# Performance work log

Measured on AMD Instinct MI355X. Metric: run time of the kernel, lower is better.

The kernel has to match this reference:

```python
import jax, jax.numpy as jnp
import numpy as np

T, B, I, H, L = 512, 64, 1024, 1024, 2


def setup_inputs() -> dict:
    key = jax.random.key(0)
    ks = jax.random.split(key, 3)
    stdv = 1.0 / np.sqrt(H)
    x = jax.random.normal(ks[0], (T, B, I), dtype=jnp.float32)
    w_ih = jax.random.uniform(ks[1], (L, 4 * H, I), dtype=jnp.float32, minval=-stdv, maxval=stdv)
    w_hh = jax.random.uniform(ks[2], (L, 4 * H, H), dtype=jnp.float32, minval=-stdv, maxval=stdv)
    b_ih = jnp.zeros((L, 4 * H), dtype=jnp.float32)
    b_hh = jnp.zeros((L, 4 * H), dtype=jnp.float32)
    h0 = jnp.zeros((L, B, H), dtype=jnp.float32)
    c0 = jnp.zeros((L, B, H), dtype=jnp.float32)
    return {"x": x, "h0": h0, "c0": c0, "w_ih": w_ih, "w_hh": w_hh, "b_ih": b_ih, "b_hh": b_hh}


def _lstm_layer(seq, h, c, w_ih_l, w_hh_l, b_ih_l, b_hh_l):
    # in2hidden: one big GEMM over all timesteps, as in the torch code
    igates = jnp.einsum('tbi,gi->tbg', seq, w_ih_l) + b_ih_l  # (T, B, 4H)

    def step(carry, ig):
        h, c = carry
        gates = ig + h @ w_hh_l.T + b_hh_l          # (B, 4H)
        i_g, f_g, g_g, o_g = jnp.split(gates, 4, axis=-1)
        c = jax.nn.sigmoid(f_g) * c + jax.nn.sigmoid(i_g) * jnp.tanh(g_g)
        h = jax.nn.sigmoid(o_g) * jnp.tanh(c)
        return (h, c), h

    (hT, cT), out = jax.lax.scan(step, (h, c), igates)
    return out, hT, cT


def reference(x, h0, c0, w_ih, w_hh, b_ih, b_hh):
    out = x
    h_fin, c_fin = [], []
    for l in range(L):  # small fixed number of structurally distinct layers
        out, hT, cT = _lstm_layer(out, h0[l], c0[l], w_ih[l], w_hh[l], b_ih[l], b_hh[l])
        h_fin.append(hT)
        c_fin.append(cT)
    return out, jnp.stack(h_fin), jnp.stack(c_fin)
```

## Files before the change

kernel.cpp:

```cpp
#include <hip/hip_runtime.h>
#include <hip/hip_bf16.h>
#include <stdint.h>

#define T_STEPS 512
#define NBATCH 64
#define HID 1024
#define NGATE 4096
#define NLAYERS 2
#define BH (NBATCH * HID)
#define TBH (T_STEPS * NBATCH * HID)
#define WEL ((size_t)NLAYERS * NGATE * HID)
#define NBLK 256

typedef __attribute__((ext_vector_type(8))) short short8;
typedef __attribute__((ext_vector_type(4))) float f32x4;

__device__ __forceinline__ ushort f2bf(float f) {
  union { float f; uint32_t i; } u; u.f = f;
  return (ushort)((u.i + 0x7fffu + ((u.i >> 16) & 1u)) >> 16);
}
__device__ __forceinline__ float bf2f(ushort b) {
  union { uint32_t i; float f; } u; u.i = ((uint32_t)b) << 16;
  return u.f;
}
__device__ __forceinline__ void gll16(const void* g, void* l) {
  __builtin_amdgcn_global_load_lds(
      (const __attribute__((address_space(1))) unsigned int*)g,
      (__attribute__((address_space(3))) unsigned int*)l, 16, 0, 0);
}

#define ISSC(SLOT, PTR, OFF) \
  asm volatile("global_load_dwordx4 %0, %1, off offset:" #OFF \
               : "=v"(fr[SLOT]) : "v"(PTR));
#define ISSU(SLOT, PTR, OFF) \
  asm volatile("global_load_dwordx4 %0, %1, off offset:" #OFF " sc0 sc1" \
               : "=v"(fr[SLOT]) : "v"(PTR));
#define VMW(N, SLOT) \
  asm volatile("s_waitcnt vmcnt(" #N ")" : "+v"(fr[SLOT]));
#define CON(SLOT, KC) { \
    const short8 b0v = *(const short8*)(bb0 + ((((KC) * 64) + kb) ^ bsw)); \
    const short8 b1v = *(const short8*)(bb1 + ((((KC) * 64) + kb) ^ bsw)); \
    accA = __builtin_amdgcn_mfma_f32_16x16x32_bf16(fr[SLOT], b0v, accA, 0, 0, 0); \
    accB = __builtin_amdgcn_mfma_f32_16x16x32_bf16(fr[SLOT], b1v, accB, 0, 0, 0); }

#define PIPE64(M0, M1) \
  M0(0,A0p,0)    M0(1,A0p,64)   M0(2,A0p,128)  M0(3,A0p,192)  \
  M0(4,A0p,256)  M0(5,A0p,320)  M0(6,A0p,384)  M0(7,A0p,448)  \
  M0(8,A0p,512)  M0(9,A0p,576)  M0(10,A0p,640) M0(11,A0p,704) \
  M0(12,A0p,768) M0(13,A0p,832) M0(14,A0p,896) M0(15,A0p,960) \
  VMW(15,0)  CON(0,0)   M0(0,A0p,1024)  \
  VMW(15,1)  CON(1,1)   M0(1,A0p,1088)  \
  VMW(15,2)  CON(2,2)   M0(2,A0p,1152)  \
  VMW(15,3)  CON(3,3)   M0(3,A0p,1216)  \
  VMW(15,4)  CON(4,4)   M0(4,A0p,1280)  \
  VMW(15,5)  CON(5,5)   M0(5,A0p,1344)  \
  VMW(15,6)  CON(6,6)   M0(6,A0p,1408)  \
  VMW(15,7)  CON(7,7)   M0(7,A0p,1472)  \
  VMW(15,8)  CON(8,8)   M0(8,A0p,1536)  \
  VMW(15,9)  CON(9,9)   M0(9,A0p,1600)  \
  VMW(15,10) CON(10,10) M0(10,A0p,1664) \
  VMW(15,11) CON(11,11) M0(11,A0p,1728) \
  VMW(15,12) CON(12,12) M0(12,A0p,1792) \
  VMW(15,13) CON(13,13) M0(13,A0p,1856) \
  VMW(15,14) CON(14,14) M0(14,A0p,1920) \
  VMW(15,15) CON(15,15) M0(15,A0p,1984) \
  VMW(15,0)  CON(0,16)  M1(0,A1p,0)     \
  VMW(15,1)  CON(1,17)  M1(1,A1p,64)    \
  VMW(15,2)  CON(2,18)  M1(2,A1p,128)   \
  VMW(15,3)  CON(3,19)  M1(3,A1p,192)   \
  VMW(15,4)  CON(4,20)  M1(4,A1p,256)   \
  VMW(15,5)  CON(5,21)  M1(5,A1p,320)   \
  VMW(15,6)  CON(6,22)  M1(6,A1p,384)   \
  VMW(15,7)  CON(7,23)  M1(7,A1p,448)   \
  VMW(15,8)  CON(8,24)  M1(8,A1p,512)   \
  VMW(15,9)  CON(9,25)  M1(9,A1p,576)   \
  VMW(15,10) CON(10,26) M1(10,A1p,640)  \
  VMW(15,11) CON(11,27) M1(11,A1p,704)  \
  VMW(15,12) CON(12,28) M1(12,A1p,768)  \
  VMW(15,13) CON(13,29) M1(13,A1p,832)  \
  VMW(15,14) CON(14,30) M1(14,A1p,896)  \
  VMW(15,15) CON(15,31) M1(15,A1p,960)  \
  VMW(15,0)  CON(0,32)  M1(0,A1p,1024)  \
  VMW(15,1)  CON(1,33)  M1(1,A1p,1088)  \
  VMW(15,2)  CON(2,34)  M1(2,A1p,1152)  \
  VMW(15,3)  CON(3,35)  M1(3,A1p,1216)  \
  VMW(15,4)  CON(4,36)  M1(4,A1p,1280)  \
  VMW(15,5)  CON(5,37)  M1(5,A1p,1344)  \
  VMW(15,6)  CON(6,38)  M1(6,A1p,1408)  \
  VMW(15,7)  CON(7,39)  M1(7,A1p,1472)  \
  VMW(15,8)  CON(8,40)  M1(8,A1p,1536)  \
  VMW(15,9)  CON(9,41)  M1(9,A1p,1600)  \
  VMW(15,10) CON(10,42) M1(10,A1p,1664) \
  VMW(15,11) CON(11,43) M1(11,A1p,1728) \
  VMW(15,12) CON(12,44) M1(12,A1p,1792) \
  VMW(15,13) CON(13,45) M1(13,A1p,1856) \
  VMW(15,14) CON(14,46) M1(14,A1p,1920) \
  VMW(15,15) CON(15,47) M1(15,A1p,1984) \
  VMW(15,0)  CON(0,48)  \
  VMW(14,1)  CON(1,49)  \
  VMW(13,2)  CON(2,50)  \
  VMW(12,3)  CON(3,51)  \
  VMW(11,4)  CON(4,52)  \
  VMW(10,5)  CON(5,53)  \
  VMW(9,6)   CON(6,54)  \
  VMW(8,7)   CON(7,55)  \
  VMW(7,8)   CON(8,56)  \
  VMW(6,9)   CON(9,57)  \
  VMW(5,10)  CON(10,58) \
  VMW(4,11)  CON(11,59) \
  VMW(3,12)  CON(12,60) \
  VMW(2,13)  CON(13,61) \
  VMW(1,14)  CON(14,62) \
  VMW(0,15)  CON(15,63)

__global__ void k_f32_to_bf16(const float* __restrict__ in, ushort* __restrict__ out, int n) {
  int i = (blockIdx.x * blockDim.x + threadIdx.x) * 4;
  if (i >= n) return;
  const float4 v = *reinterpret_cast<const float4*>(in + i);
  ushort4 o; o.x = f2bf(v.x); o.y = f2bf(v.y); o.z = f2bf(v.z); o.w = f2bf(v.w);
  *reinterpret_cast<ushort4*>(out + i) = o;
}
__global__ void k_zero(int* p, int n) {
  int i = blockIdx.x * blockDim.x + threadIdx.x;
  if (i < n) p[i] = 0;
}

struct ScanP {
  const ushort* wih; const ushort* whh;
  const ushort* xb;  const ushort* hinit;
  ushort* h0r;
  ushort* h1d;
  const float* c0; const float* bi; const float* bh;
  float* out; int* bar;
};

__device__ __forceinline__ void gbar(int* bar, int phase, int stripe, bool isRoot) {
  __syncthreads();
  if (threadIdx.x == 0) {
    __hip_atomic_fetch_add(bar + stripe * 16, 1, __ATOMIC_RELAXED, __HIP_MEMORY_SCOPE_AGENT);
    if (isRoot) {
      const int target = (phase + 1) * NBLK;
      for (;;) {
        int sum = 0;
#pragma unroll
        for (int i = 0; i < 16; ++i)
          sum += __hip_atomic_load(bar + i * 16, __ATOMIC_RELAXED, __HIP_MEMORY_SCOPE_AGENT);
        if (sum >= target) break;
        __builtin_amdgcn_s_sleep(1);
      }
      __hip_atomic_store(bar + 256, phase + 1, __ATOMIC_RELAXED, __HIP_MEMORY_SCOPE_AGENT);
    } else {
      while (__hip_atomic_load(bar + 256, __ATOMIC_RELAXED, __HIP_MEMORY_SCOPE_AGENT) < phase + 1)
        __builtin_amdgcn_s_sleep(4);
    }
  }
  __syncthreads();
  __builtin_amdgcn_sched_barrier(0);
}

__global__ __launch_bounds__(256, 1) void k_scan(ScanP p) {
  __shared__ __align__(16) ushort Wl[32 * 2048];
  __shared__ float glds[64 * 33];
  const int tid = threadIdx.x, wave = tid >> 6, lane = tid & 63;
  const bool isL1 = blockIdx.x >= 128;
  const int cb = isL1 ? (int)blockIdx.x - 128 : (int)blockIdx.x;
  const int j0 = cb * 8;
  const int stripe = blockIdx.x & 15;
  const bool isRoot = (blockIdx.x == 0);

  const ushort* wihL = p.wih + (isL1 ? (size_t)NGATE * HID : 0);
  const ushort* whhL = p.whh + (isL1 ? (size_t)NGATE * HID : 0);
  for (int q = wave; q < 128; q += 4) {
    const int i = q >> 2, ch = q & 3;
    const ushort* base = (ch < 2) ? wihL : whhL;
    const int g = (i >> 3) * 1024 + j0 + (i & 7);
    gll16(base + (size_t)g * 1024 + (ch & 1) * 512 + (((lane * 16) ^ ((i & 7) << 4)) >> 1),
          (char*)Wl + i * 4096 + ch * 1024);
  }

  const int eb  = tid >> 2;
  const int jl0 = (tid & 3) * 2;
  const int jj  = j0 + jl0;
  const int lofs = isL1 ? NGATE : 0;
  float creg[2], bias[4][2];
#pragma unroll
  for (int i = 0; i < 2; ++i) creg[i] = p.c0[(isL1 ? BH : 0) + eb * 1024 + jj + i];
#pragma unroll
  for (int g = 0; g < 4; ++g)
#pragma unroll
    for (int i = 0; i < 2; ++i)
      bias[g][i] = p.bi[lofs + g * 1024 + jj + i] + p.bh[lofs + g * 1024 + jj + i];

  const size_t aoff = (size_t)(wave * 16 + (lane & 15)) * 1024 + (size_t)((lane >> 4) * 8);
  const int r0 = lane & 15;
  const char* bb0 = (const char*)Wl + r0 * 4096;
  const char* bb1 = (const char*)Wl + (r0 + 16) * 4096;
  const int bsw = (r0 & 7) << 4;
  const int kb = (lane >> 4) * 16;

  __syncthreads();

  for (int s = 0; s < T_STEPS + 1; ++s) {
    const bool act = isL1 ? (s >= 1) : (s < T_STEPS);
    if (act) {
      f32x4 accA = {0.f, 0.f, 0.f, 0.f}, accB = {0.f, 0.f, 0.f, 0.f};
      short8 fr[16];
      if (!isL1) {
        const ushort* A0p = p.xb + (size_t)s * BH + aoff;
        const ushort* A1p = ((s == 0) ? p.hinit : p.h0r + (size_t)(s - 1) * BH) + aoff;
        PIPE64(ISSC, ISSC)
      } else {
        const ushort* A0p = p.h0r + (size_t)(s - 1) * BH + aoff;
        const ushort* A1p = ((s == 1) ? p.hinit + BH : p.h1d + (size_t)(s & 1) * BH) + aoff;
        PIPE64(ISSC, ISSU)
      }
#pragma unroll
      for (int r = 0; r < 4; ++r) {
        const int row = wave * 16 + (lane >> 4) * 4 + r;
        glds[row * 33 + r0]      = accA[r];
        glds[row * 33 + 16 + r0] = accB[r];
      }
      __syncthreads();

      float hres[2];
#pragma unroll
      for (int i = 0; i < 2; ++i) {
        const int jl = jl0 + i;
        const float gi = glds[eb * 33 + jl]      + bias[0][i];
        const float gf = glds[eb * 33 + 8 + jl]  + bias[1][i];
        const float gg = glds[eb * 33 + 16 + jl] + bias[2][i];
        const float go = glds[eb * 33 + 24 + jl] + bias[3][i];
        float c = creg[i];
        const float si = 1.f / (1.f + __expf(-gi));
        const float sf = 1.f / (1.f + __expf(-gf));
        const float so = 1.f / (1.f + __expf(-go));
        const float tg = tanhf(gg);
        c = sf * c + si * tg;
        hres[i] = so * tanhf(c);
        creg[i] = c;
      }

      const uint32_t packed = (uint32_t)f2bf(hres[0]) | ((uint32_t)f2bf(hres[1]) << 16);
      ushort* hdst = (!isL1) ? (p.h0r + (size_t)s * BH)
                             : (p.h1d + (size_t)((s - 1) & 1) * BH);
      uint32_t* hw = (uint32_t*)(hdst + eb * 1024 + jj);
      __hip_atomic_store(hw, packed, __ATOMIC_RELAXED, __HIP_MEMORY_SCOPE_AGENT);
      uint32_t chk = __hip_atomic_load(hw, __ATOMIC_RELAXED, __HIP_MEMORY_SCOPE_AGENT);
      asm volatile("" :: "v"(chk));

      if (isL1) {
#pragma unroll
        for (int i = 0; i < 2; ++i)
          p.out[(size_t)(s - 1) * BH + eb * 1024 + jj + i] = hres[i];
        if (s - 1 == T_STEPS - 1) {
#pragma unroll
          for (int i = 0; i < 2; ++i) {
            p.out[(size_t)TBH + BH + eb * 1024 + jj + i] = hres[i];
            p.out[(size_t)TBH + 3 * BH + eb * 1024 + jj + i] = creg[i];
          }
        }
      } else if (s == T_STEPS - 1) {
#pragma unroll
        for (int i = 0; i < 2; ++i) {
          p.out[(size_t)TBH + eb * 1024 + jj + i] = hres[i];
          p.out[(size_t)TBH + 2 * BH + eb * 1024 + jj + i] = creg[i];
        }
      }
    }
    gbar(p.bar, s, stripe, isRoot);
  }
}

extern "C" void kernel_launch(void* const* d_in, const int* in_sizes, int n_in,
                              void* d_out, int out_size, void* d_ws, size_t ws_size,
                              hipStream_t stream) {
  const float* x    = (const float*)d_in[0];
  const float* h0   = (const float*)d_in[1];
  const float* c0   = (const float*)d_in[2];
  const float* w_ih = (const float*)d_in[3];
  const float* w_hh = (const float*)d_in[4];
  const float* b_ih = (const float*)d_in[5];
  const float* b_hh = (const float*)d_in[6];
  float* out = (float*)d_out;

  ushort* xb    = (ushort*)d_ws;
  ushort* wihb  = xb + (size_t)TBH;
  ushort* whhb  = wihb + WEL;
  ushort* hinit = whhb + WEL;
  ushort* h0r   = hinit + 2 * (size_t)BH;
  ushort* h1d   = h0r + (size_t)TBH;
  int*    bar   = (int*)(h1d + 2 * (size_t)BH);

  const size_t need = ((size_t)2 * TBH + 2 * WEL + 4 * (size_t)BH) * 2 + 4096;
  if (ws_size < need) return;

  { int n = TBH;        k_f32_to_bf16<<<(n / 4 + 255) / 256, 256, 0, stream>>>(x, xb, n); }
  { int n = (int)WEL;   k_f32_to_bf16<<<(n / 4 + 255) / 256, 256, 0, stream>>>(w_ih, wihb, n); }
  { int n = (int)WEL;   k_f32_to_bf16<<<(n / 4 + 255) / 256, 256, 0, stream>>>(w_hh, whhb, n); }
  { int n = 2 * BH;     k_f32_to_bf16<<<(n / 4 + 255) / 256, 256, 0, stream>>>(h0, hinit, n); }
  k_zero<<<2, 256, 0, stream>>>(bar, 512);

  ScanP sp;
  sp.wih = wihb; sp.whh = whhb;
  sp.xb = xb; sp.hinit = hinit;
  sp.h0r = h0r; sp.h1d = h1d;
  sp.c0 = c0; sp.bi = b_ih; sp.bh = b_hh;
  sp.out = out; sp.bar = bar;

  void* kp[1] = {&sp};
  hipLaunchCooperativeKernel(reinterpret_cast<void*>(&k_scan),
                             dim3(NBLK), dim3(256), kp, 0, stream);
}
```

Before: 5.995 ms.

## Split K across eight waves with register-resident weights and LDS reduction

Changes the persistent cooperative LSTM scan from 4 waves that split the batch rows to 8 waves that split the K dimension: four waves take the input/lower-layer K range and four take the recurrent K range, each in 256-element chunks. Each wave keeps its slice of the weight tile in registers instead of LDS. The per-wave partial gate sums are then reduced through LDS before the elementwise cell update. The intent is to halve each wave's serial load/MFMA chain per step and drop the LDS weight reads, at the cost of more register pressure, an 8-way LDS reduction, and one thread per output with shuffle packing. The barrier spin sleep is also shortened.

```diff
diff --git a/kernel.cpp b/kernel.cpp
--- a/kernel.cpp
+++ b/kernel.cpp
@@ -19,99 +19,56 @@
   union { float f; uint32_t i; } u; u.f = f;
   return (ushort)((u.i + 0x7fffu + ((u.i >> 16) & 1u)) >> 16);
 }
-__device__ __forceinline__ float bf2f(ushort b) {
-  union { uint32_t i; float f; } u; u.i = ((uint32_t)b) << 16;
-  return u.f;
-}
-__device__ __forceinline__ void gll16(const void* g, void* l) {
-  __builtin_amdgcn_global_load_lds(
-      (const __attribute__((address_space(1))) unsigned int*)g,
-      (__attribute__((address_space(3))) unsigned int*)l, 16, 0, 0);
-}
-
-#define ISSC(SLOT, PTR, OFF) \
+
+#define ISSC(S, M, OFF) \
   asm volatile("global_load_dwordx4 %0, %1, off offset:" #OFF \
-               : "=v"(fr[SLOT]) : "v"(PTR));
-#define ISSU(SLOT, PTR, OFF) \
+               : "=v"(fr[S]) : "v"(aP[M]));
+#define ISSU(S, M, OFF) \
   asm volatile("global_load_dwordx4 %0, %1, off offset:" #OFF " sc0 sc1" \
-               : "=v"(fr[SLOT]) : "v"(PTR));
+               : "=v"(fr[S]) : "v"(aP[M]));
 #define VMW(N, SLOT) \
   asm volatile("s_waitcnt vmcnt(" #N ")" : "+v"(fr[SLOT]));
-#define CON(SLOT, KC) { \
-    const short8 b0v = *(const short8*)(bb0 + ((((KC) * 64) + kb) ^ bsw)); \
-    const short8 b1v = *(const short8*)(bb1 + ((((KC) * 64) + kb) ^ bsw)); \
-    accA = __builtin_amdgcn_mfma_f32_16x16x32_bf16(fr[SLOT], b0v, accA, 0, 0, 0); \
-    accB = __builtin_amdgcn_mfma_f32_16x16x32_bf16(fr[SLOT], b1v, accB, 0, 0, 0); }
-
-#define PIPE64(M0, M1) \
-  M0(0,A0p,0)    M0(1,A0p,64)   M0(2,A0p,128)  M0(3,A0p,192)  \
-  M0(4,A0p,256)  M0(5,A0p,320)  M0(6,A0p,384)  M0(7,A0p,448)  \
-  M0(8,A0p,512)  M0(9,A0p,576)  M0(10,A0p,640) M0(11,A0p,704) \
-  M0(12,A0p,768) M0(13,A0p,832) M0(14,A0p,896) M0(15,A0p,960) \
-  VMW(15,0)  CON(0,0)   M0(0,A0p,1024)  \
-  VMW(15,1)  CON(1,1)   M0(1,A0p,1088)  \
-  VMW(15,2)  CON(2,2)   M0(2,A0p,1152)  \
-  VMW(15,3)  CON(3,3)   M0(3,A0p,1216)  \
-  VMW(15,4)  CON(4,4)   M0(4,A0p,1280)  \
-  VMW(15,5)  CON(5,5)   M0(5,A0p,1344)  \
-  VMW(15,6)  CON(6,6)   M0(6,A0p,1408)  \
-  VMW(15,7)  CON(7,7)   M0(7,A0p,1472)  \
-  VMW(15,8)  CON(8,8)   M0(8,A0p,1536)  \
-  VMW(15,9)  CON(9,9)   M0(9,A0p,1600)  \
-  VMW(15,10) CON(10,10) M0(10,A0p,1664) \
-  VMW(15,11) CON(11,11) M0(11,A0p,1728) \
-  VMW(15,12) CON(12,12) M0(12,A0p,1792) \
-  VMW(15,13) CON(13,13) M0(13,A0p,1856) \
-  VMW(15,14) CON(14,14) M0(14,A0p,1920) \
-  VMW(15,15) CON(15,15) M0(15,A0p,1984) \
-  VMW(15,0)  CON(0,16)  M1(0,A1p,0)     \
-  VMW(15,1)  CON(1,17)  M1(1,A1p,64)    \
-  VMW(15,2)  CON(2,18)  M1(2,A1p,128)   \
-  VMW(15,3)  CON(3,19)  M1(3,A1p,192)   \
-  VMW(15,4)  CON(4,20)  M1(4,A1p,256)   \
-  VMW(15,5)  CON(5,21)  M1(5,A1p,320)   \
-  VMW(15,6)  CON(6,22)  M1(6,A1p,384)   \
-  VMW(15,7)  CON(7,23)  M1(7,A1p,448)   \
-  VMW(15,8)  CON(8,24)  M1(8,A1p,512)   \
-  VMW(15,9)  CON(9,25)  M1(9,A1p,576)   \
-  VMW(15,10) CON(10,26) M1(10,A1p,640)  \
-  VMW(15,11) CON(11,27) M1(11,A1p,704)  \
-  VMW(15,12) CON(12,28) M1(12,A1p,768)  \
-  VMW(15,13) CON(13,29) M1(13,A1p,832)  \
-  VMW(15,14) CON(14,30) M1(14,A1p,896)  \
-  VMW(15,15) CON(15,31) M1(15,A1p,960)  \
-  VMW(15,0)  CON(0,32)  M1(0,A1p,1024)  \
-  VMW(15,1)  CON(1,33)  M1(1,A1p,1088)  \
-  VMW(15,2)  CON(2,34)  M1(2,A1p,1152)  \
-  VMW(15,3)  CON(3,35)  M1(3,A1p,1216)  \
-  VMW(15,4)  CON(4,36)  M1(4,A1p,1280)  \
-  VMW(15,5)  CON(5,37)  M1(5,A1p,1344)  \
-  VMW(15,6)  CON(6,38)  M1(6,A1p,1408)  \
-  VMW(15,7)  CON(7,39)  M1(7,A1p,1472)  \
-  VMW(15,8)  CON(8,40)  M1(8,A1p,1536)  \
-  VMW(15,9)  CON(9,41)  M1(9,A1p,1600)  \
-  VMW(15,10) CON(10,42) M1(10,A1p,1664) \
-  VMW(15,11) CON(11,43) M1(11,A1p,1728) \
-  VMW(15,12) CON(12,44) M1(12,A1p,1792) \
-  VMW(15,13) CON(13,45) M1(13,A1p,1856) \
-  VMW(15,14) CON(14,46) M1(14,A1p,1920) \
-  VMW(15,15) CON(15,47) M1(15,A1p,1984) \
-  VMW(15,0)  CON(0,48)  \
-  VMW(14,1)  CON(1,49)  \
-  VMW(13,2)  CON(2,50)  \
-  VMW(12,3)  CON(3,51)  \
-  VMW(11,4)  CON(4,52)  \
-  VMW(10,5)  CON(5,53)  \
-  VMW(9,6)   CON(6,54)  \
-  VMW(8,7)   CON(7,55)  \
-  VMW(7,8)   CON(8,56)  \
-  VMW(6,9)   CON(9,57)  \
-  VMW(5,10)  CON(10,58) \
-  VMW(4,11)  CON(11,59) \
-  VMW(3,12)  CON(12,60) \
-  VMW(2,13)  CON(13,61) \
-  VMW(1,14)  CON(14,62) \
-  VMW(0,15)  CON(15,63)
+#define CON(S, M, KC) { \
+    accA[M] = __builtin_amdgcn_mfma_f32_16x16x32_bf16(fr[S], breg[0][KC], accA[M], 0, 0, 0); \
+    accB[M] = __builtin_amdgcn_mfma_f32_16x16x32_bf16(fr[S], breg[1][KC], accB[M], 0, 0, 0); }
+
+#define PIPE(I) \
+  I(0,0,0)    I(1,1,0)    I(2,2,0)    I(3,3,0)   \
+  I(4,0,64)   I(5,1,64)   I(6,2,64)   I(7,3,64)  \
+  I(8,0,128)  I(9,1,128)  I(10,2,128) I(11,3,128)\
+  I(12,0,192) I(13,1,192) I(14,2,192) I(15,3,192)\
+  VMW(15,0)  CON(0,0,0)  I(0,0,256)  \
+  VMW(15,1)  CON(1,1,0)  I(1,1,256)  \
+  VMW(15,2)  CON(2,2,0)  I(2,2,256)  \
+  VMW(15,3)  CON(3,3,0)  I(3,3,256)  \
+  VMW(15,4)  CON(4,0,1)  I(4,0,320)  \
+  VMW(15,5)  CON(5,1,1)  I(5,1,320)  \
+  VMW(15,6)  CON(6,2,1)  I(6,2,320)  \
+  VMW(15,7)  CON(7,3,1)  I(7,3,320)  \
+  VMW(15,8)  CON(8,0,2)  I(8,0,384)  \
+  VMW(15,9)  CON(9,1,2)  I(9,1,384)  \
+  VMW(15,10) CON(10,2,2) I(10,2,384) \
+  VMW(15,11) CON(11,3,2) I(11,3,384) \
+  VMW(15,12) CON(12,0,3) I(12,0,448) \
+  VMW(15,13) CON(13,1,3) I(13,1,448) \
+  VMW(15,14) CON(14,2,3) I(14,2,448) \
+  VMW(15,15) CON(15,3,3) I(15,3,448) \
+  VMW(15,0)  CON(0,0,4)  \
+  VMW(14,1)  CON(1,1,4)  \
+  VMW(13,2)  CON(2,2,4)  \
+  VMW(12,3)  CON(3,3,4)  \
+  VMW(11,4)  CON(4,0,5)  \
+  VMW(10,5)  CON(5,1,5)  \
+  VMW(9,6)   CON(6,2,5)  \
+  VMW(8,7)   CON(7,3,5)  \
+  VMW(7,8)   CON(8,0,6)  \
+  VMW(6,9)   CON(9,1,6)  \
+  VMW(5,10)  CON(10,2,6) \
+  VMW(4,11)  CON(11,3,6) \
+  VMW(3,12)  CON(12,0,7) \
+  VMW(2,13)  CON(13,1,7) \
+  VMW(1,14)  CON(14,2,7) \
+  VMW(0,15)  CON(15,3,7)
 
 __global__ void k_f32_to_bf16(const float* __restrict__ in, ushort* __restrict__ out, int n) {
   int i = (blockIdx.x * blockDim.x + threadIdx.x) * 4;
@@ -151,120 +108,114 @@
       __hip_atomic_store(bar + 256, phase + 1, __ATOMIC_RELAXED, __HIP_MEMORY_SCOPE_AGENT);
     } else {
       while (__hip_atomic_load(bar + 256, __ATOMIC_RELAXED, __HIP_MEMORY_SCOPE_AGENT) < phase + 1)
-        __builtin_amdgcn_s_sleep(4);
+        __builtin_amdgcn_s_sleep(2);
     }
   }
   __syncthreads();
   __builtin_amdgcn_sched_barrier(0);
 }
 
-__global__ __launch_bounds__(256, 1) void k_scan(ScanP p) {
-  __shared__ __align__(16) ushort Wl[32 * 2048];
-  __shared__ float glds[64 * 33];
+__global__ __launch_bounds__(512, 1) void k_scan(ScanP p) {
+  __shared__ float glds[8][32][68];
   const int tid = threadIdx.x, wave = tid >> 6, lane = tid & 63;
   const bool isL1 = blockIdx.x >= 128;
   const int cb = isL1 ? (int)blockIdx.x - 128 : (int)blockIdx.x;
   const int j0 = cb * 8;
   const int stripe = blockIdx.x & 15;
   const bool isRoot = (blockIdx.x == 0);
+  const bool hiSrc = wave >= 4;
+  const int koff = (wave & 3) * 256;
 
   const ushort* wihL = p.wih + (isL1 ? (size_t)NGATE * HID : 0);
   const ushort* whhL = p.whh + (isL1 ? (size_t)NGATE * HID : 0);
-  for (int q = wave; q < 128; q += 4) {
-    const int i = q >> 2, ch = q & 3;
-    const ushort* base = (ch < 2) ? wihL : whhL;
+  const ushort* bsrc = hiSrc ? whhL : wihL;
+  short8 breg[2][8];
+#pragma unroll
+  for (int t = 0; t < 2; ++t) {
+    const int i = t * 16 + (lane & 15);
     const int g = (i >> 3) * 1024 + j0 + (i & 7);
-    gll16(base + (size_t)g * 1024 + (ch & 1) * 512 + (((lane * 16) ^ ((i & 7) << 4)) >> 1),
-          (char*)Wl + i * 4096 + ch * 1024);
+    const ushort* bp = bsrc + (size_t)g * 1024 + koff + (lane >> 4) * 8;
+#pragma unroll
+    for (int kc = 0; kc < 8; ++kc) breg[t][kc] = *(const short8*)(bp + kc * 32);
   }
 
-  const int eb  = tid >> 2;
-  const int jl0 = (tid & 3) * 2;
-  const int jj  = j0 + jl0;
+  const int eb = tid >> 3, jl = tid & 7, jj = j0 + jl;
   const int lofs = isL1 ? NGATE : 0;
-  float creg[2], bias[4][2];
-#pragma unroll
-  for (int i = 0; i < 2; ++i) creg[i] = p.c0[(isL1 ? BH : 0) + eb * 1024 + jj + i];
+  float creg = p.c0[(isL1 ? BH : 0) + eb * 1024 + jj];
+  float bias[4];
 #pragma unroll
   for (int g = 0; g < 4; ++g)
-#pragma unroll
-    for (int i = 0; i < 2; ++i)
-      bias[g][i] = p.bi[lofs + g * 1024 + jj + i] + p.bh[lofs + g * 1024 + jj + i];
-
-  const size_t aoff = (size_t)(wave * 16 + (lane & 15)) * 1024 + (size_t)((lane >> 4) * 8);
-  const int r0 = lane & 15;
-  const char* bb0 = (const char*)Wl + r0 * 4096;
-  const char* bb1 = (const char*)Wl + (r0 + 16) * 4096;
-  const int bsw = (r0 & 7) << 4;
-  const int kb = (lane >> 4) * 16;
-
-  __syncthreads();
+    bias[g] = p.bi[lofs + g * 1024 + jj] + p.bh[lofs + g * 1024 + jj];
+
+  const size_t arow = (size_t)(lane & 15) * 1024 + koff + (lane >> 4) * 8;
 
   for (int s = 0; s < T_STEPS + 1; ++s) {
     const bool act = isL1 ? (s >= 1) : (s < T_STEPS);
     if (act) {
-      f32x4 accA = {0.f, 0.f, 0.f, 0.f}, accB = {0.f, 0.f, 0.f, 0.f};
+      const ushort* src;
+      if (!isL1) src = hiSrc ? ((s == 0) ? p.hinit : p.h0r + (size_t)(s - 1) * BH)
+                             : (p.xb + (size_t)s * BH);
+      else       src = hiSrc ? ((s == 1) ? p.hinit + BH : p.h1d + (size_t)(s & 1) * BH)
+                             : (p.h0r + (size_t)(s - 1) * BH);
+      const ushort* base = src + arow;
+      const ushort* aP[4] = { base, base + 16 * 1024, base + 32 * 1024, base + 48 * 1024 };
+      f32x4 accA[4], accB[4];
+#pragma unroll
+      for (int m = 0; m < 4; ++m) {
+        accA[m] = (f32x4){0.f, 0.f, 0.f, 0.f};
+        accB[m] = (f32x4){0.f, 0.f, 0.f, 0.f};
+      }
       short8 fr[16];
-      if (!isL1) {
-        const ushort* A0p = p.xb + (size_t)s * BH + aoff;
-        const ushort* A1p = ((s == 0) ? p.hinit : p.h0r + (size_t)(s - 1) * BH) + aoff;
-        PIPE64(ISSC, ISSC)
-      } else {
-        const ushort* A0p = p.h0r + (size_t)(s - 1) * BH + aoff;
-        const ushort* A1p = ((s == 1) ? p.hinit + BH : p.h1d + (size_t)(s & 1) * BH) + aoff;
-        PIPE64(ISSC, ISSU)
-      }
-#pragma unroll
-      for (int r = 0; r < 4; ++r) {
-        const int row = wave * 16 + (lane >> 4) * 4 + r;
-        glds[row * 33 + r0]      = accA[r];
-        glds[row * 33 + 16 + r0] = accB[r];
+      if (isL1 && hiSrc) { PIPE(ISSU) } else { PIPE(ISSC) }
+
+      {
+        const int r0 = lane & 15, q4 = (lane >> 4) * 4;
+#pragma unroll
+        for (int m = 0; m < 4; ++m) {
+          *(f32x4*)&glds[wave][r0][m * 16 + q4]      = accA[m];
+          *(f32x4*)&glds[wave][16 + r0][m * 16 + q4] = accB[m];
+        }
       }
       __syncthreads();
 
-      float hres[2];
-#pragma unroll
-      for (int i = 0; i < 2; ++i) {
-        const int jl = jl0 + i;
-        const float gi = glds[eb * 33 + jl]      + bias[0][i];
-        const float gf = glds[eb * 33 + 8 + jl]  + bias[1][i];
-        const float gg = glds[eb * 33 + 16 + jl] + bias[2][i];
-        const float go = glds[eb * 33 + 24 + jl] + bias[3][i];
-        float c = creg[i];
-        const float si = 1.f / (1.f + __expf(-gi));
-        const float sf = 1.f / (1.f + __expf(-gf));
-        const float so = 1.f / (1.f + __expf(-go));
-        const float tg = tanhf(gg);
-        c = sf * c + si * tg;
-        hres[i] = so * tanhf(c);
-        creg[i] = c;
-      }
-
-      const uint32_t packed = (uint32_t)f2bf(hres[0]) | ((uint32_t)f2bf(hres[1]) << 16);
+      float v[4];
+#pragma unroll
+      for (int g = 0; g < 4; ++g) {
+        float t = bias[g];
+#pragma unroll
+        for (int w = 0; w < 8; ++w) t += glds[w][g * 8 + jl][eb];
+        v[g] = t;
+      }
+      float c = creg;
+      const float si = 1.f / (1.f + __expf(-v[0]));
+      const float sf = 1.f / (1.f + __expf(-v[1]));
+      const float tg = tanhf(v[2]);
+      const float so = 1.f / (1.f + __expf(-v[3]));
+      c = sf * c + si * tg;
+      const float h = so * tanhf(c);
+      creg = c;
+
+      const uint32_t hu = (uint32_t)f2bf(h);
+      const uint32_t other = __shfl_xor(hu, 1);
       ushort* hdst = (!isL1) ? (p.h0r + (size_t)s * BH)
                              : (p.h1d + (size_t)((s - 1) & 1) * BH);
-      uint32_t* hw = (uint32_t*)(hdst + eb * 1024 + jj);
-      __hip_atomic_store(hw, packed, __ATOMIC_RELAXED, __HIP_MEMORY_SCOPE_AGENT);
-      uint32_t chk = __hip_atomic_load(hw, __ATOMIC_RELAXED, __HIP_MEMORY_SCOPE_AGENT);
-      asm volatile("" :: "v"(chk));
+      if (!(tid & 1)) {
+        uint32_t* hw = (uint32_t*)(hdst + eb * 1024 + jj);
+        const uint32_t packed = hu | (other << 16);
+        __hip_atomic_store(hw, packed, __ATOMIC_RELAXED, __HIP_MEMORY_SCOPE_AGENT);
+        uint32_t chk = __hip_atomic_load(hw, __ATOMIC_RELAXED, __HIP_MEMORY_SCOPE_AGENT);
+        asm volatile("" :: "v"(chk));
+      }
 
       if (isL1) {
-#pragma unroll
-        for (int i = 0; i < 2; ++i)
-          p.out[(size_t)(s - 1) * BH + eb * 1024 + jj + i] = hres[i];
+        p.out[(size_t)(s - 1) * BH + eb * 1024 + jj] = h;
         if (s - 1 == T_STEPS - 1) {
-#pragma unroll
-          for (int i = 0; i < 2; ++i) {
-            p.out[(size_t)TBH + BH + eb * 1024 + jj + i] = hres[i];
-            p.out[(size_t)TBH + 3 * BH + eb * 1024 + jj + i] = creg[i];
-          }
+          p.out[(size_t)TBH + BH + eb * 1024 + jj] = h;
+          p.out[(size_t)TBH + 3 * BH + eb * 1024 + jj] = c;
         }
       } else if (s == T_STEPS - 1) {
-#pragma unroll
-        for (int i = 0; i < 2; ++i) {
-          p.out[(size_t)TBH + eb * 1024 + jj + i] = hres[i];
-          p.out[(size_t)TBH + 2 * BH + eb * 1024 + jj + i] = creg[i];
-        }
+        p.out[(size_t)TBH + eb * 1024 + jj] = h;
+        p.out[(size_t)TBH + 2 * BH + eb * 1024 + jj] = c;
       }
     }
     gbar(p.bar, s, stripe, isRoot);
@@ -309,5 +260,5 @@
 
   void* kp[1] = {&sp};
   hipLaunchCooperativeKernel(reinterpret_cast<void*>(&k_scan),
-                             dim3(NBLK), dim3(256), kp, 0, stream);
-}
+                             dim3(NBLK), dim3(512), kp, 0, stream);
+}
```

Measured after the change: 6.865 ms. 1.15x slower.

## Decouple layer barriers so layer 1 trails layer 0 via release flag

Applied to the files above, without the earlier changes.

Replaces the single grid-wide barrier shared by both layers with two independent 128-block barriers, one per layer. Layer 1 blocks now wait only on layer 0's release counter for step t and no longer hold layer 0 back, so layer 0 can run ahead. Layer 1 hidden states go to a full T-length buffer instead of a double buffer, which uses more workspace but avoids write-after-read hazards now that the layers are no longer in lockstep. The uncached sc0 sc1 load variant for layer-1 hidden state is dropped, since each step reads from a fresh buffer slot.

```diff
diff --git a/kernel.cpp b/kernel.cpp
--- a/kernel.cpp
+++ b/kernel.cpp
@@ -10,7 +10,7 @@
 #define BH (NBATCH * HID)
 #define TBH (T_STEPS * NBATCH * HID)
 #define WEL ((size_t)NLAYERS * NGATE * HID)
-#define NBLK 256
+#define GBLK 128
 
 typedef __attribute__((ext_vector_type(8))) short short8;
 typedef __attribute__((ext_vector_type(4))) float f32x4;
@@ -18,10 +18,6 @@
 __device__ __forceinline__ ushort f2bf(float f) {
   union { float f; uint32_t i; } u; u.f = f;
   return (ushort)((u.i + 0x7fffu + ((u.i >> 16) & 1u)) >> 16);
-}
-__device__ __forceinline__ float bf2f(ushort b) {
-  union { uint32_t i; float f; } u; u.i = ((uint32_t)b) << 16;
-  return u.f;
 }
 __device__ __forceinline__ void gll16(const void* g, void* l) {
   __builtin_amdgcn_global_load_lds(
@@ -29,12 +25,9 @@
       (__attribute__((address_space(3))) unsigned int*)l, 16, 0, 0);
 }
 
-#define ISSC(SLOT, PTR, OFF) \
+#define ISSC(S, P, OFF) \
   asm volatile("global_load_dwordx4 %0, %1, off offset:" #OFF \
-               : "=v"(fr[SLOT]) : "v"(PTR));
-#define ISSU(SLOT, PTR, OFF) \
-  asm volatile("global_load_dwordx4 %0, %1, off offset:" #OFF " sc0 sc1" \
-               : "=v"(fr[SLOT]) : "v"(PTR));
+               : "=v"(fr[S]) : "v"(P));
 #define VMW(N, SLOT) \
   asm volatile("s_waitcnt vmcnt(" #N ")" : "+v"(fr[SLOT]));
 #define CON(SLOT, KC) { \
@@ -43,59 +36,59 @@
     accA = __builtin_amdgcn_mfma_f32_16x16x32_bf16(fr[SLOT], b0v, accA, 0, 0, 0); \
     accB = __builtin_amdgcn_mfma_f32_16x16x32_bf16(fr[SLOT], b1v, accB, 0, 0, 0); }
 
-#define PIPE64(M0, M1) \
-  M0(0,A0p,0)    M0(1,A0p,64)   M0(2,A0p,128)  M0(3,A0p,192)  \
-  M0(4,A0p,256)  M0(5,A0p,320)  M0(6,A0p,384)  M0(7,A0p,448)  \
-  M0(8,A0p,512)  M0(9,A0p,576)  M0(10,A0p,640) M0(11,A0p,704) \
-  M0(12,A0p,768) M0(13,A0p,832) M0(14,A0p,896) M0(15,A0p,960) \
-  VMW(15,0)  CON(0,0)   M0(0,A0p,1024)  \
-  VMW(15,1)  CON(1,1)   M0(1,A0p,1088)  \
-  VMW(15,2)  CON(2,2)   M0(2,A0p,1152)  \
-  VMW(15,3)  CON(3,3)   M0(3,A0p,1216)  \
-  VMW(15,4)  CON(4,4)   M0(4,A0p,1280)  \
-  VMW(15,5)  CON(5,5)   M0(5,A0p,1344)  \
-  VMW(15,6)  CON(6,6)   M0(6,A0p,1408)  \
-  VMW(15,7)  CON(7,7)   M0(7,A0p,1472)  \
-  VMW(15,8)  CON(8,8)   M0(8,A0p,1536)  \
-  VMW(15,9)  CON(9,9)   M0(9,A0p,1600)  \
-  VMW(15,10) CON(10,10) M0(10,A0p,1664) \
-  VMW(15,11) CON(11,11) M0(11,A0p,1728) \
-  VMW(15,12) CON(12,12) M0(12,A0p,1792) \
-  VMW(15,13) CON(13,13) M0(13,A0p,1856) \
-  VMW(15,14) CON(14,14) M0(14,A0p,1920) \
-  VMW(15,15) CON(15,15) M0(15,A0p,1984) \
-  VMW(15,0)  CON(0,16)  M1(0,A1p,0)     \
-  VMW(15,1)  CON(1,17)  M1(1,A1p,64)    \
-  VMW(15,2)  CON(2,18)  M1(2,A1p,128)   \
-  VMW(15,3)  CON(3,19)  M1(3,A1p,192)   \
-  VMW(15,4)  CON(4,20)  M1(4,A1p,256)   \
-  VMW(15,5)  CON(5,21)  M1(5,A1p,320)   \
-  VMW(15,6)  CON(6,22)  M1(6,A1p,384)   \
-  VMW(15,7)  CON(7,23)  M1(7,A1p,448)   \
-  VMW(15,8)  CON(8,24)  M1(8,A1p,512)   \
-  VMW(15,9)  CON(9,25)  M1(9,A1p,576)   \
-  VMW(15,10) CON(10,26) M1(10,A1p,640)  \
-  VMW(15,11) CON(11,27) M1(11,A1p,704)  \
-  VMW(15,12) CON(12,28) M1(12,A1p,768)  \
-  VMW(15,13) CON(13,29) M1(13,A1p,832)  \
-  VMW(15,14) CON(14,30) M1(14,A1p,896)  \
-  VMW(15,15) CON(15,31) M1(15,A1p,960)  \
-  VMW(15,0)  CON(0,32)  M1(0,A1p,1024)  \
-  VMW(15,1)  CON(1,33)  M1(1,A1p,1088)  \
-  VMW(15,2)  CON(2,34)  M1(2,A1p,1152)  \
-  VMW(15,3)  CON(3,35)  M1(3,A1p,1216)  \
-  VMW(15,4)  CON(4,36)  M1(4,A1p,1280)  \
-  VMW(15,5)  CON(5,37)  M1(5,A1p,1344)  \
-  VMW(15,6)  CON(6,38)  M1(6,A1p,1408)  \
-  VMW(15,7)  CON(7,39)  M1(7,A1p,1472)  \
-  VMW(15,8)  CON(8,40)  M1(8,A1p,1536)  \
-  VMW(15,9)  CON(9,41)  M1(9,A1p,1600)  \
-  VMW(15,10) CON(10,42) M1(10,A1p,1664) \
-  VMW(15,11) CON(11,43) M1(11,A1p,1728) \
-  VMW(15,12) CON(12,44) M1(12,A1p,1792) \
-  VMW(15,13) CON(13,45) M1(13,A1p,1856) \
-  VMW(15,14) CON(14,46) M1(14,A1p,1920) \
-  VMW(15,15) CON(15,47) M1(15,A1p,1984) \
+#define PIPE64() \
+  ISSC(0,A0p,0)    ISSC(1,A0p,64)   ISSC(2,A0p,128)  ISSC(3,A0p,192)  \
+  ISSC(4,A0p,256)  ISSC(5,A0p,320)  ISSC(6,A0p,384)  ISSC(7,A0p,448)  \
+  ISSC(8,A0p,512)  ISSC(9,A0p,576)  ISSC(10,A0p,640) ISSC(11,A0p,704) \
+  ISSC(12,A0p,768) ISSC(13,A0p,832) ISSC(14,A0p,896) ISSC(15,A0p,960) \
+  VMW(15,0)  CON(0,0)   ISSC(0,A0p,1024)  \
+  VMW(15,1)  CON(1,1)   ISSC(1,A0p,1088)  \
+  VMW(15,2)  CON(2,2)   ISSC(2,A0p,1152)  \
+  VMW(15,3)  CON(3,3)   ISSC(3,A0p,1216)  \
+  VMW(15,4)  CON(4,4)   ISSC(4,A0p,1280)  \
+  VMW(15,5)  CON(5,5)   ISSC(5,A0p,1344)  \
+  VMW(15,6)  CON(6,6)   ISSC(6,A0p,1408)  \
+  VMW(15,7)  CON(7,7)   ISSC(7,A0p,1472)  \
+  VMW(15,8)  CON(8,8)   ISSC(8,A0p,1536)  \
+  VMW(15,9)  CON(9,9)   ISSC(9,A0p,1600)  \
+  VMW(15,10) CON(10,10) ISSC(10,A0p,1664) \
+  VMW(15,11) CON(11,11) ISSC(11,A0p,1728) \
+  VMW(15,12) CON(12,12) ISSC(12,A0p,1792) \
+  VMW(15,13) CON(13,13) ISSC(13,A0p,1856) \
+  VMW(15,14) CON(14,14) ISSC(14,A0p,1920) \
+  VMW(15,15) CON(15,15) ISSC(15,A0p,1984) \
+  VMW(15,0)  CON(0,16)  ISSC(0,A1p,0)     \
+  VMW(15,1)  CON(1,17)  ISSC(1,A1p,64)    \
+  VMW(15,2)  CON(2,18)  ISSC(2,A1p,128)   \
+  VMW(15,3)  CON(3,19)  ISSC(3,A1p,192)   \
+  VMW(15,4)  CON(4,20)  ISSC(4,A1p,256)   \
+  VMW(15,5)  CON(5,21)  ISSC(5,A1p,320)   \
+  VMW(15,6)  CON(6,22)  ISSC(6,A1p,384)   \
+  VMW(15,7)  CON(7,23)  ISSC(7,A1p,448)   \
+  VMW(15,8)  CON(8,24)  ISSC(8,A1p,512)   \
+  VMW(15,9)  CON(9,25)  ISSC(9,A1p,576)   \
+  VMW(15,10) CON(10,26) ISSC(10,A1p,640)  \
+  VMW(15,11) CON(11,27) ISSC(11,A1p,704)  \
+  VMW(15,12) CON(12,28) ISSC(12,A1p,768)  \
+  VMW(15,13) CON(13,29) ISSC(13,A1p,832)  \
+  VMW(15,14) CON(14,30) ISSC(14,A1p,896)  \
+  VMW(15,15) CON(15,31) ISSC(15,A1p,960)  \
+  VMW(15,0)  CON(0,32)  ISSC(0,A1p,1024)  \
+  VMW(15,1)  CON(1,33)  ISSC(1,A1p,1088)  \
+  VMW(15,2)  CON(2,34)  ISSC(2,A1p,1152)  \
+  VMW(15,3)  CON(3,35)  ISSC(3,A1p,1216)  \
+  VMW(15,4)  CON(4,36)  ISSC(4,A1p,1280)  \
+  VMW(15,5)  CON(5,37)  ISSC(5,A1p,1344)  \
+  VMW(15,6)  CON(6,38)  ISSC(6,A1p,1408)  \
+  VMW(15,7)  CON(7,39)  ISSC(7,A1p,1472)  \
+  VMW(15,8)  CON(8,40)  ISSC(8,A1p,1536)  \
+  VMW(15,9)  CON(9,41)  ISSC(9,A1p,1600)  \
+  VMW(15,10) CON(10,42) ISSC(10,A1p,1664) \
+  VMW(15,11) CON(11,43) ISSC(11,A1p,1728) \
+  VMW(15,12) CON(12,44) ISSC(12,A1p,1792) \
+  VMW(15,13) CON(13,45) ISSC(13,A1p,1856) \
+  VMW(15,14) CON(14,46) ISSC(14,A1p,1920) \
+  VMW(15,15) CON(15,47) ISSC(15,A1p,1984) \
   VMW(15,0)  CON(0,48)  \
   VMW(14,1)  CON(1,49)  \
   VMW(13,2)  CON(2,50)  \
@@ -129,29 +122,29 @@
   const ushort* wih; const ushort* whh;
   const ushort* xb;  const ushort* hinit;
   ushort* h0r;
-  ushort* h1d;
+  ushort* h1r;
   const float* c0; const float* bi; const float* bh;
   float* out; int* bar;
 };
 
-__device__ __forceinline__ void gbar(int* bar, int phase, int stripe, bool isRoot) {
+__device__ __forceinline__ void gbar(int* gb, int phase, int stripe, bool isRoot) {
   __syncthreads();
   if (threadIdx.x == 0) {
-    __hip_atomic_fetch_add(bar + stripe * 16, 1, __ATOMIC_RELAXED, __HIP_MEMORY_SCOPE_AGENT);
+    __hip_atomic_fetch_add(gb + stripe * 16, 1, __ATOMIC_RELAXED, __HIP_MEMORY_SCOPE_AGENT);
     if (isRoot) {
-      const int target = (phase + 1) * NBLK;
+      const int target = (phase + 1) * GBLK;
       for (;;) {
         int sum = 0;
 #pragma unroll
         for (int i = 0; i < 16; ++i)
-          sum += __hip_atomic_load(bar + i * 16, __ATOMIC_RELAXED, __HIP_MEMORY_SCOPE_AGENT);
+          sum += __hip_atomic_load(gb + i * 16, __ATOMIC_RELAXED, __HIP_MEMORY_SCOPE_AGENT);
         if (sum >= target) break;
         __builtin_amdgcn_s_sleep(1);
       }
-      __hip_atomic_store(bar + 256, phase + 1, __ATOMIC_RELAXED, __HIP_MEMORY_SCOPE_AGENT);
+      __hip_atomic_store(gb + 256, phase + 1, __ATOMIC_RELAXED, __HIP_MEMORY_SCOPE_AGENT);
     } else {
-      while (__hip_atomic_load(bar + 256, __ATOMIC_RELAXED, __HIP_MEMORY_SCOPE_AGENT) < phase + 1)
-        __builtin_amdgcn_s_sleep(4);
+      while (__hip_atomic_load(gb + 256, __ATOMIC_RELAXED, __HIP_MEMORY_SCOPE_AGENT) < phase + 1)
+        __builtin_amdgcn_s_sleep(2);
     }
   }
   __syncthreads();
@@ -165,8 +158,10 @@
   const bool isL1 = blockIdx.x >= 128;
   const int cb = isL1 ? (int)blockIdx.x - 128 : (int)blockIdx.x;
   const int j0 = cb * 8;
-  const int stripe = blockIdx.x & 15;
-  const bool isRoot = (blockIdx.x == 0);
+  const int stripe = cb & 15;
+  const bool isRoot = (cb == 0);
+  int* gb = p.bar + (isL1 ? 512 : 0);
+  int* rel0 = p.bar + 256;
 
   const ushort* wihL = p.wih + (isL1 ? (size_t)NGATE * HID : 0);
   const ushort* whhL = p.whh + (isL1 ? (size_t)NGATE * HID : 0);
@@ -200,74 +195,83 @@
 
   __syncthreads();
 
-  for (int s = 0; s < T_STEPS + 1; ++s) {
-    const bool act = isL1 ? (s >= 1) : (s < T_STEPS);
-    if (act) {
-      f32x4 accA = {0.f, 0.f, 0.f, 0.f}, accB = {0.f, 0.f, 0.f, 0.f};
-      short8 fr[16];
+  for (int t = 0; t < T_STEPS; ++t) {
+    if (isL1) {
+      if (threadIdx.x == 0) {
+        while (__hip_atomic_load(rel0, __ATOMIC_RELAXED, __HIP_MEMORY_SCOPE_AGENT) < t + 1)
+          __builtin_amdgcn_s_sleep(2);
+      }
+      __syncthreads();
+      __builtin_amdgcn_sched_barrier(0);
+    }
+
+    f32x4 accA = {0.f, 0.f, 0.f, 0.f}, accB = {0.f, 0.f, 0.f, 0.f};
+    short8 fr[16];
+    {
+      const ushort* A0p;
+      const ushort* A1p;
       if (!isL1) {
-        const ushort* A0p = p.xb + (size_t)s * BH + aoff;
-        const ushort* A1p = ((s == 0) ? p.hinit : p.h0r + (size_t)(s - 1) * BH) + aoff;
-        PIPE64(ISSC, ISSC)
+        A0p = p.xb + (size_t)t * BH + aoff;
+        A1p = ((t == 0) ? p.hinit : p.h0r + (size_t)(t - 1) * BH) + aoff;
       } else {
-        const ushort* A0p = p.h0r + (size_t)(s - 1) * BH + aoff;
-        const ushort* A1p = ((s == 1) ? p.hinit + BH : p.h1d + (size_t)(s & 1) * BH) + aoff;
-        PIPE64(ISSC, ISSU)
-      }
-#pragma unroll
-      for (int r = 0; r < 4; ++r) {
-        const int row = wave * 16 + (lane >> 4) * 4 + r;
-        glds[row * 33 + r0]      = accA[r];
-        glds[row * 33 + 16 + r0] = accB[r];
-      }
-      __syncthreads();
-
-      float hres[2];
+        A0p = p.h0r + (size_t)t * BH + aoff;
+        A1p = ((t == 0) ? p.hinit + BH : p.h1r + (size_t)(t - 1) * BH) + aoff;
+      }
+      PIPE64()
+    }
+#pragma unroll
+    for (int r = 0; r < 4; ++r) {
+      const int row = wave * 16 + (lane >> 4) * 4 + r;
+      glds[row * 33 + r0]      = accA[r];
+      glds[row * 33 + 16 + r0] = accB[r];
+    }
+    __syncthreads();
+
+    float hres[2];
+#pragma unroll
+    for (int i = 0; i < 2; ++i) {
+      const int jl = jl0 + i;
+      const float gi = glds[eb * 33 + jl]      + bias[0][i];
+      const float gf = glds[eb * 33 + 8 + jl]  + bias[1][i];
+      const float gg = glds[eb * 33 + 16 + jl] + bias[2][i];
+      const float go = glds[eb * 33 + 24 + jl] + bias[3][i];
+      float c = creg[i];
+      const float si = 1.f / (1.f + __expf(-gi));
+      const float sf = 1.f / (1.f + __expf(-gf));
+      const float so = 1.f / (1.f + __expf(-go));
+      const float tg = tanhf(gg);
+      c = sf * c + si * tg;
+      hres[i] = so * tanhf(c);
+      creg[i] = c;
+    }
+
+    const uint32_t packed = (uint32_t)f2bf(hres[0]) | ((uint32_t)f2bf(hres[1]) << 16);
+    ushort* hdst = (!isL1) ? (p.h0r + (size_t)t * BH) : (p.h1r + (size_t)t * BH);
+    uint32_t* hw = (uint32_t*)(hdst + eb * 1024 + jj);
+    __hip_atomic_store(hw, packed, __ATOMIC_RELAXED, __HIP_MEMORY_SCOPE_AGENT);
+    uint32_t chk = __hip_atomic_load(hw, __ATOMIC_RELAXED, __HIP_MEMORY_SCOPE_AGENT);
+    asm volatile("" :: "v"(chk));
+
+    if (isL1) {
+#pragma unroll
+      for (int i = 0; i < 2; ++i)
+        p.out[(size_t)t * BH + eb * 1024 + jj + i] = hres[i];
+      if (t == T_STEPS - 1) {
+#pragma unroll
+        for (int i = 0; i < 2; ++i) {
+          p.out[(size_t)TBH + BH + eb * 1024 + jj + i] = hres[i];
+          p.out[(size_t)TBH + 3 * BH + eb * 1024 + jj + i] = creg[i];
+        }
+      }
+    } else if (t == T_STEPS - 1) {
 #pragma unroll
       for (int i = 0; i < 2; ++i) {
-        const int jl = jl0 + i;
-        const float gi = glds[eb * 33 + jl]      + bias[0][i];
-        const float gf = glds[eb * 33 + 8 + jl]  + bias[1][i];
-        const float gg = glds[eb * 33 + 16 + jl] + bias[2][i];
-        const float go = glds[eb * 33 + 24 + jl] + bias[3][i];
-        float c = creg[i];
-        const float si = 1.f / (1.f + __expf(-gi));
-        const float sf = 1.f / (1.f + __expf(-gf));
-        const float so = 1.f / (1.f + __expf(-go));
-        const float tg = tanhf(gg);
-        c = sf * c + si * tg;
-        hres[i] = so * tanhf(c);
-        creg[i] = c;
-      }
-
-      const uint32_t packed = (uint32_t)f2bf(hres[0]) | ((uint32_t)f2bf(hres[1]) << 16);
-      ushort* hdst = (!isL1) ? (p.h0r + (size_t)s * BH)
-                             : (p.h1d + (size_t)((s - 1) & 1) * BH);
-      uint32_t* hw = (uint32_t*)(hdst + eb * 1024 + jj);
-      __hip_atomic_store(hw, packed, __ATOMIC_RELAXED, __HIP_MEMORY_SCOPE_AGENT);
-      uint32_t chk = __hip_atomic_load(hw, __ATOMIC_RELAXED, __HIP_MEMORY_SCOPE_AGENT);
-      asm volatile("" :: "v"(chk));
-
-      if (isL1) {
-#pragma unroll
-        for (int i = 0; i < 2; ++i)
-          p.out[(size_t)(s - 1) * BH + eb * 1024 + jj + i] = hres[i];
-        if (s - 1 == T_STEPS - 1) {
-#pragma unroll
-          for (int i = 0; i < 2; ++i) {
-            p.out[(size_t)TBH + BH + eb * 1024 + jj + i] = hres[i];
-            p.out[(size_t)TBH + 3 * BH + eb * 1024 + jj + i] = creg[i];
-          }
-        }
-      } else if (s == T_STEPS - 1) {
-#pragma unroll
-        for (int i = 0; i < 2; ++i) {
-          p.out[(size_t)TBH + eb * 1024 + jj + i] = hres[i];
-          p.out[(size_t)TBH + 2 * BH + eb * 1024 + jj + i] = creg[i];
-        }
-      }
-    }
-    gbar(p.bar, s, stripe, isRoot);
+        p.out[(size_t)TBH + eb * 1024 + jj + i] = hres[i];
+        p.out[(size_t)TBH + 2 * BH + eb * 1024 + jj + i] = creg[i];
+      }
+    }
+
+    gbar(gb, t, stripe, isRoot);
   }
 }
 
@@ -288,26 +292,26 @@
   ushort* whhb  = wihb + WEL;
   ushort* hinit = whhb + WEL;
   ushort* h0r   = hinit + 2 * (size_t)BH;
-  ushort* h1d   = h0r + (size_t)TBH;
-  int*    bar   = (int*)(h1d + 2 * (size_t)BH);
-
-  const size_t need = ((size_t)2 * TBH + 2 * WEL + 4 * (size_t)BH) * 2 + 4096;
+  ushort* h1r   = h0r + (size_t)TBH;
+  int*    bar   = (int*)(h1r + (size_t)TBH);
+
+  const size_t need = ((size_t)3 * TBH + 2 * WEL + 2 * (size_t)BH) * 2 + 4096;
   if (ws_size < need) return;
 
   { int n = TBH;        k_f32_to_bf16<<<(n / 4 + 255) / 256, 256, 0, stream>>>(x, xb, n); }
   { int n = (int)WEL;   k_f32_to_bf16<<<(n / 4 + 255) / 256, 256, 0, stream>>>(w_ih, wihb, n); }
   { int n = (int)WEL;   k_f32_to_bf16<<<(n / 4 + 255) / 256, 256, 0, stream>>>(w_hh, whhb, n); }
   { int n = 2 * BH;     k_f32_to_bf16<<<(n / 4 + 255) / 256, 256, 0, stream>>>(h0, hinit, n); }
-  k_zero<<<2, 256, 0, stream>>>(bar, 512);
+  k_zero<<<4, 256, 0, stream>>>(bar, 1024);
 
   ScanP sp;
   sp.wih = wihb; sp.whh = whhb;
   sp.xb = xb; sp.hinit = hinit;
-  sp.h0r = h0r; sp.h1d = h1d;
+  sp.h0r = h0r; sp.h1r = h1r;
   sp.c0 = c0; sp.bi = b_ih; sp.bh = b_hh;
   sp.out = out; sp.bar = bar;
 
   void* kp[1] = {&sp};
   hipLaunchCooperativeKernel(reinterpret_cast<void*>(&k_scan),
-                             dim3(NBLK), dim3(256), kp, 0, stream);
-}
+                             dim3(256), dim3(256), kp, 0, stream);
+}
```

Measured after the change: 6.001 ms. Within noise of the previous version (+0.1%).
